# Kernel tuning notes

Hardware: AMD Instinct MI355X
Metric: run time of the kernel (lower is better)

## Reference

```python
import jax, jax.numpy as jnp
import numpy as np

M, N = 4096, 4096
N_COEF = 768
ALPHA = 16.0


def _dct_mat(K):
    # Orthonormal DCT-II matrix D: D[k, t] = s(k) * cos(pi * (t + 0.5) * k / K)
    # dct2d(X)  = D_M @ X @ D_N.T ;  idct2d(Y) = D_M.T @ Y @ D_N  (DCT-III)
    k = jnp.arange(K, dtype=jnp.float32)[:, None]
    t = jnp.arange(K, dtype=jnp.float32)[None, :]
    D = jnp.cos(jnp.pi * (t + 0.5) * k / K)
    scale = jnp.where(k == 0, jnp.sqrt(1.0 / K), jnp.sqrt(2.0 / K))
    return (D * scale).astype(jnp.float32)


def setup_inputs() -> dict:
    key = jax.random.key(0)
    k1, k2, k3 = jax.random.split(key, 3)
    weight = jax.random.normal(k1, (M, N), dtype=jnp.float32) * 0.02
    dW_params = jax.random.normal(k2, (N_COEF,), dtype=jnp.float32) * 0.05
    flat_indices = jax.random.randint(k3, (N_COEF,), 0, M * N, dtype=jnp.int64)
    return {"weight": weight, "dW_params": dW_params, "flat_indices": flat_indices}


def reference(weight, dW_params, flat_indices):
    # W_eff = stop_grad(W) + idct2d(scatter(dW_params)) * alpha
    m, n = weight.shape
    dW_F = jnp.zeros(m * n, dtype=jnp.float32).at[flat_indices].set(dW_params)
    dW_F = dW_F.reshape(m, n)
    D_M = _dct_mat(m)
    D_N = _dct_mat(n)
    dW_T = D_M.T @ dW_F @ D_N  # dense 2D inverse DCT (DCT-III)
    return jax.lax.stop_gradient(weight) + dW_T * ALPHA
```

## Files before the change

kernel.cpp:

```cpp
#include <hip/hip_runtime.h>

#define MDIM 4096
#define NDIM 4096
#define NCOEF 768
#define ALPHA 16.0f
#define PANEL_U16 (96 * 256 * 8)

typedef __attribute__((ext_vector_type(8))) short bf16x8;
typedef __attribute__((ext_vector_type(4))) float f32x4;

__device__ __forceinline__ unsigned short f2bf(float x) {
    unsigned u = __float_as_uint(x);
    u += 0x7FFFu + ((u >> 16) & 1u);
    return (unsigned short)(u >> 16);
}

__device__ __forceinline__ void glds16(const unsigned short* src, unsigned short* dst) {
    __builtin_amdgcn_global_load_lds(
        (const __attribute__((address_space(1))) void*)src,
        (__attribute__((address_space(3))) void*)dst, 16, 0, 0);
}

__global__ __launch_bounds__(256) void fill_uv(
    const int* __restrict__ fidx, const float* __restrict__ dw,
    unsigned short* __restrict__ U, unsigned short* __restrict__ V)
{
    __shared__ int idx_s[NCOEF];
    __shared__ int dup[8];
    const int b = blockIdx.x;
    const int half = b & 1;
    const int pk = b >> 1;
    const int panel = pk / 96;
    const int kc = pk - panel * 96;
    const int t = threadIdx.x;
    #pragma unroll
    for (int j = 0; j < 3; ++j) idx_s[t + (j << 8)] = fidx[t + (j << 8)];
    if (t < 8) dup[t] = 0;
    __syncthreads();
    {
        const int ci = t >> 5;
        const int pci = (kc << 3) + ci;
        const int myidx = idx_s[pci];
        const int q0 = (t & 31) * 24;
        int found = 0;
        #pragma unroll
        for (int s = 0; s < 24; ++s) {
            const int q = q0 + s;
            found |= (q > pci) & (idx_s[q] == myidx);
        }
        if (found) dup[ci] = 1;
    }
    __syncthreads();
    const int rl = (half << 7) + (t >> 1);
    const int row = (panel << 8) + rl;
    const int p0 = (kc << 3) + ((t & 1) << 2);
    const unsigned tt = 2u * (unsigned)row + 1u;
    const float wrev = 1.0f / 16384.0f;
    const float s0 = 0.015625f;
    const float s1 = 0.022097086912079612f;
    unsigned short uo[4], vo[4];
    #pragma unroll
    for (int j = 0; j < 4; ++j) {
        const int p = p0 + j;
        const int idx = idx_s[p];
        const int r = idx >> 12;
        const int c = idx & (NDIM - 1);
        const float su = (r == 0) ? s0 : s1;
        const float sv = (dup[p - (kc << 3)] ? 0.0f : 1.0f) * ALPHA * dw[p]
                         * ((c == 0) ? s0 : s1);
        const unsigned nu = (tt * (unsigned)r) & 16383u;
        const unsigned nv = (tt * (unsigned)c) & 16383u;
        uo[j] = f2bf(su * __builtin_amdgcn_cosf((float)nu * wrev));
        vo[j] = f2bf(sv * __builtin_amdgcn_cosf((float)nv * wrev));
    }
    const size_t o = ((size_t)pk * 256 + rl) * 8 + ((t & 1) << 2);
    *(ushort4*)(U + o) = *(const ushort4*)uo;
    *(ushort4*)(V + o) = *(const ushort4*)vo;
}

__global__ __launch_bounds__(512, 1) void gemm_kernel(
    const float* __restrict__ W,
    const unsigned short* __restrict__ U,
    const unsigned short* __restrict__ V,
    float* __restrict__ out)
{
    __shared__ unsigned short SM[65536];
    unsigned short* const As = SM;
    unsigned short* const Bs = SM + 32768;

    const int tid = threadIdx.x;
    const int lane = tid & 63;
    const int wave = tid >> 6;

    const int bid = blockIdx.x;
    const int xcd = bid & 7;
    const int local = bid >> 3;
    const int by = ((xcd >> 1) << 2) + (local >> 3);
    const int bx = ((xcd & 1) << 3) + (local & 7);
    const int wr = wave >> 2;
    const int wc = wave & 3;
    const int fr = lane & 15;
    const int fks = lane >> 4;

    const unsigned short* uPan = U + (size_t)by * PANEL_U16;
    const unsigned short* vPan = V + (size_t)bx * PANEL_U16;

    f32x4 acc[8][4] = {};

    const int aO = (((fks << 8) + wr * 128 + fr) << 3);
    const int bO = (((fks << 8) + wc * 64 + fr) << 3);

    const int bcol = (bx << 8) + (lane << 2);
    const int erowBase = (by << 8);
    float4 wA[2][4];
    float4 wB[2][4];

#define STAGE(j, buf) do {                                                  \
        const unsigned short* uS = uPan + (size_t)(j) * 8192;               \
        const unsigned short* vS = vPan + (size_t)(j) * 8192;               \
        glds16(uS + ((size_t)tid << 3),        &As[(buf) * 8192 + (wave << 9)]); \
        glds16(uS + 4096 + ((size_t)tid << 3), &As[(buf) * 8192 + 4096 + (wave << 9)]); \
        glds16(vS + ((size_t)tid << 3),        &Bs[(buf) * 8192 + (wave << 9)]); \
        glds16(vS + 4096 + ((size_t)tid << 3), &Bs[(buf) * 8192 + 4096 + (wave << 9)]); \
    } while (0)

#define COMPUTE(buf) do {                                                   \
        bf16x8 a[8], b[4];                                                  \
        _Pragma("unroll")                                                   \
        for (int fm = 0; fm < 8; ++fm)                                      \
            a[fm] = *(const bf16x8*)&As[(buf) * 8192 + aO + (fm << 7)];     \
        _Pragma("unroll")                                                   \
        for (int fn = 0; fn < 4; ++fn)                                      \
            b[fn] = *(const bf16x8*)&Bs[(buf) * 8192 + bO + (fn << 7)];     \
        _Pragma("unroll")                                                   \
        for (int fm = 0; fm < 8; ++fm)                                      \
            _Pragma("unroll")                                               \
            for (int fn = 0; fn < 4; ++fn)                                  \
                acc[fm][fn] = __builtin_amdgcn_mfma_f32_16x16x32_bf16(      \
                    b[fn], a[fm], acc[fm][fn], 0, 0, 0);                    \
    } while (0)

    STAGE(0, 0);
    STAGE(1, 1);
    #pragma unroll
    for (int j = 0; j < 24; ++j) {
        if (j < 22) STAGE(j + 2, (j + 2) & 3);
        if (j == 21) {
            #pragma unroll
            for (int cc = 0; cc < 2; ++cc)
                #pragma unroll
                for (int i = 0; i < 4; ++i)
                    wA[cc][i] = *(const float4*)(
                        W + (size_t)(erowBase + cc * 32 + wave * 4 + i) * NDIM + bcol);
        }
        if (j < 21)       asm volatile("s_waitcnt vmcnt(8)"  ::: "memory");
        else if (j == 21) asm volatile("s_waitcnt vmcnt(16)" ::: "memory");
        else if (j == 22) asm volatile("s_waitcnt vmcnt(12)" ::: "memory");
        else              asm volatile("s_waitcnt vmcnt(8)"  ::: "memory");
        __builtin_amdgcn_s_barrier();
        asm volatile("" ::: "memory");
        COMPUTE(j & 3);
    }

    float* const L = (float*)SM;
    if (wr == 0) {
        #pragma unroll
        for (int f2 = 0; f2 < 2; ++f2)
            #pragma unroll
            for (int fn = 0; fn < 4; ++fn)
                *(f32x4*)(L + (f2 * 16 + fr) * 258 + wc * 64 + fn * 16 + fks * 4)
                    = acc[f2][fn];
    }
    #pragma unroll
    for (int c = 0; c < 8; ++c) {
        asm volatile("s_waitcnt lgkmcnt(0)" ::: "memory");
        __builtin_amdgcn_s_barrier();
        asm volatile("" ::: "memory");
        if (c < 7) {
            if (wr == ((c + 1) >> 2)) {
                #pragma unroll
                for (int f2 = 0; f2 < 2; ++f2)
                    #pragma unroll
                    for (int fn = 0; fn < 4; ++fn)
                        *(f32x4*)(L + ((c + 1) & 1) * 8256
                                  + (f2 * 16 + fr) * 258 + wc * 64 + fn * 16 + fks * 4)
                            = acc[((c + 1) & 3) * 2 + f2][fn];
            }
        }
        #pragma unroll
        for (int i = 0; i < 4; ++i) {
            const int rl2 = wave * 4 + i;
            const size_t o = (size_t)(erowBase + c * 32 + rl2) * NDIM + bcol;
            const f32x4 l4 = *(const f32x4*)(L + (c & 1) * 8256 + rl2 * 258 + (lane << 2));
            const float4 w4 = (c < 2) ? wA[c][i] : wB[c & 1][i];
            float4 r4;
            r4.x = w4.x + l4[0];
            r4.y = w4.y + l4[1];
            r4.z = w4.z + l4[2];
            r4.w = w4.w + l4[3];
            *(float4*)(out + o) = r4;
        }
        if (c < 6) {
            #pragma unroll
            for (int i = 0; i < 4; ++i)
                wB[c & 1][i] = *(const float4*)(
                    W + (size_t)(erowBase + (c + 2) * 32 + wave * 4 + i) * NDIM + bcol);
        }
    }
#undef STAGE
#undef COMPUTE
}

extern "C" void kernel_launch(void* const* d_in, const int* in_sizes, int n_in,
                              void* d_out, int out_size, void* d_ws, size_t ws_size,
                              hipStream_t stream) {
    const float* weight = (const float*)d_in[0];
    const float* dw     = (const float*)d_in[1];
    const int*   fidx   = (const int*)d_in[2];
    float* out = (float*)d_out;

    char* ws = (char*)d_ws;
    unsigned short* U = (unsigned short*)ws;
    unsigned short* V = (unsigned short*)(ws + 6291456);

    fill_uv<<<16 * 96 * 2, 256, 0, stream>>>(fidx, weight ? (const float*)d_in[1] : (const float*)d_in[1], U, V);
    gemm_kernel<<<256, 512, 0, stream>>>(weight, U, V, out);
}
```

Before: 51.29 us.

## Split GEMM tiles to 256x128 with two blocks per CU and double buffering

The GEMM kernel now uses 256-thread blocks on 256x128 output tiles instead of 512-thread blocks on 256x256, with 512 blocks launched and two blocks per CU. LDS is cut to double buffering (from quad) so that two blocks fit, and an extra barrier per k-step is added. The epilogue is restructured to stage one 32-row chunk at a time, with W prefetch reorganized across threads. This aims to raise occupancy and improve load balance, at the cost of more barriers, less prefetch depth and more redundant U loads across blocks.

After: 48.89 us. 1.05x faster.

```diff
diff --git a/kernel.cpp b/kernel.cpp
--- a/kernel.cpp
+++ b/kernel.cpp
@@ -78,15 +78,15 @@
     *(ushort4*)(V + o) = *(const ushort4*)vo;
 }
 
-__global__ __launch_bounds__(512, 1) void gemm_kernel(
+__global__ __launch_bounds__(256, 2) void gemm_kernel(
     const float* __restrict__ W,
     const unsigned short* __restrict__ U,
     const unsigned short* __restrict__ V,
     float* __restrict__ out)
 {
-    __shared__ unsigned short SM[65536];
+    __shared__ unsigned short SM[24576];
     unsigned short* const As = SM;
-    unsigned short* const Bs = SM + 32768;
+    unsigned short* const Bs = SM + 16384;
 
     const int tid = threadIdx.x;
     const int lane = tid & 63;
@@ -95,116 +95,121 @@
     const int bid = blockIdx.x;
     const int xcd = bid & 7;
     const int local = bid >> 3;
-    const int by = ((xcd >> 1) << 2) + (local >> 3);
-    const int bx = ((xcd & 1) << 3) + (local & 7);
-    const int wr = wave >> 2;
-    const int wc = wave & 3;
+    const int by = ((xcd >> 1) << 2) + (local >> 4);
+    const int bx = ((xcd & 1) << 4) + (local & 15);
+    const int wr = wave >> 1;
+    const int wc = wave & 1;
     const int fr = lane & 15;
     const int fks = lane >> 4;
 
     const unsigned short* uPan = U + (size_t)by * PANEL_U16;
-    const unsigned short* vPan = V + (size_t)bx * PANEL_U16;
+    const unsigned short* vBase = V + (size_t)(bx >> 1) * PANEL_U16
+                                    + (size_t)(bx & 1) * 1024;
 
     f32x4 acc[8][4] = {};
 
     const int aO = (((fks << 8) + wr * 128 + fr) << 3);
-    const int bO = (((fks << 8) + wc * 64 + fr) << 3);
-
-    const int bcol = (bx << 8) + (lane << 2);
-    const int erowBase = (by << 8);
-    float4 wA[2][4];
-    float4 wB[2][4];
-
-#define STAGE(j, buf) do {                                                  \
-        const unsigned short* uS = uPan + (size_t)(j) * 8192;               \
-        const unsigned short* vS = vPan + (size_t)(j) * 8192;               \
-        glds16(uS + ((size_t)tid << 3),        &As[(buf) * 8192 + (wave << 9)]); \
-        glds16(uS + 4096 + ((size_t)tid << 3), &As[(buf) * 8192 + 4096 + (wave << 9)]); \
-        glds16(vS + ((size_t)tid << 3),        &Bs[(buf) * 8192 + (wave << 9)]); \
-        glds16(vS + 4096 + ((size_t)tid << 3), &Bs[(buf) * 8192 + 4096 + (wave << 9)]); \
+    const int bO = (((fks << 7) + wc * 64 + fr) << 3);
+
+    const int bcol = bx << 7;
+    const int erowBase = by << 8;
+    float4 wpre[2][4];
+
+#define STAGE(j, buf) do {                                                   \
+        const unsigned short* uS = uPan + (size_t)(j) * 8192;                \
+        const unsigned short* vS = vBase + (size_t)(j) * 8192;               \
+        _Pragma("unroll")                                                    \
+        for (int q = 0; q < 4; ++q)                                          \
+            glds16(uS + (((q << 8) + tid) << 3),                             \
+                   &As[(buf) * 8192 + ((q << 11) + (wave << 9))]);           \
+        _Pragma("unroll")                                                    \
+        for (int q = 0; q < 2; ++q) {                                        \
+            const int c = (q << 8) + tid;                                    \
+            glds16(vS + ((c + ((c >> 7) << 7)) << 3),                        \
+                   &Bs[(buf) * 4096 + ((q << 11) + (wave << 9))]);           \
+        }                                                                    \
     } while (0)
 
-#define COMPUTE(buf) do {                                                   \
-        bf16x8 a[8], b[4];                                                  \
-        _Pragma("unroll")                                                   \
-        for (int fm = 0; fm < 8; ++fm)                                      \
-            a[fm] = *(const bf16x8*)&As[(buf) * 8192 + aO + (fm << 7)];     \
-        _Pragma("unroll")                                                   \
-        for (int fn = 0; fn < 4; ++fn)                                      \
-            b[fn] = *(const bf16x8*)&Bs[(buf) * 8192 + bO + (fn << 7)];     \
-        _Pragma("unroll")                                                   \
-        for (int fm = 0; fm < 8; ++fm)                                      \
-            _Pragma("unroll")                                               \
-            for (int fn = 0; fn < 4; ++fn)                                  \
-                acc[fm][fn] = __builtin_amdgcn_mfma_f32_16x16x32_bf16(      \
-                    b[fn], a[fm], acc[fm][fn], 0, 0, 0);                    \
+#define COMPUTE(buf) do {                                                    \
+        bf16x8 a[8], b[4];                                                   \
+        _Pragma("unroll")                                                    \
+        for (int fm = 0; fm < 8; ++fm)                                       \
+            a[fm] = *(const bf16x8*)&As[(buf) * 8192 + aO + (fm << 7)];      \
+        _Pragma("unroll")                                                    \
+        for (int fn = 0; fn < 4; ++fn)                                       \
+            b[fn] = *(const bf16x8*)&Bs[(buf) * 4096 + bO + (fn << 7)];      \
+        _Pragma("unroll")                                                    \
+        for (int fm = 0; fm < 8; ++fm)                                       \
+            _Pragma("unroll")                                                \
+            for (int fn = 0; fn < 4; ++fn)                                   \
+                acc[fm][fn] = __builtin_amdgcn_mfma_f32_16x16x32_bf16(       \
+                    b[fn], a[fm], acc[fm][fn], 0, 0, 0);                     \
     } while (0)
 
     STAGE(0, 0);
-    STAGE(1, 1);
     #pragma unroll
     for (int j = 0; j < 24; ++j) {
-        if (j < 22) STAGE(j + 2, (j + 2) & 3);
-        if (j == 21) {
+        if (j < 23) STAGE(j + 1, (j + 1) & 1);
+        if (j == 22) {
             #pragma unroll
-            for (int cc = 0; cc < 2; ++cc)
-                #pragma unroll
-                for (int i = 0; i < 4; ++i)
-                    wA[cc][i] = *(const float4*)(
-                        W + (size_t)(erowBase + cc * 32 + wave * 4 + i) * NDIM + bcol);
-        }
-        if (j < 21)       asm volatile("s_waitcnt vmcnt(8)"  ::: "memory");
-        else if (j == 21) asm volatile("s_waitcnt vmcnt(16)" ::: "memory");
-        else if (j == 22) asm volatile("s_waitcnt vmcnt(12)" ::: "memory");
-        else              asm volatile("s_waitcnt vmcnt(8)"  ::: "memory");
+            for (int i = 0; i < 4; ++i) {
+                const int idx = (i << 8) + tid;
+                wpre[0][i] = *(const float4*)(
+                    W + (size_t)(erowBase + (idx >> 5)) * NDIM + bcol + ((idx & 31) << 2));
+            }
+        }
+        if (j < 22)       asm volatile("s_waitcnt vmcnt(6)"  ::: "memory");
+        else if (j == 22) asm volatile("s_waitcnt vmcnt(10)" ::: "memory");
+        else              asm volatile("s_waitcnt vmcnt(4)"  ::: "memory");
         __builtin_amdgcn_s_barrier();
         asm volatile("" ::: "memory");
-        COMPUTE(j & 3);
+        COMPUTE(j & 1);
+        if (j < 23) {
+            asm volatile("s_waitcnt lgkmcnt(0)" ::: "memory");
+            __builtin_amdgcn_s_barrier();
+            asm volatile("" ::: "memory");
+        }
     }
 
     float* const L = (float*)SM;
-    if (wr == 0) {
-        #pragma unroll
-        for (int f2 = 0; f2 < 2; ++f2)
-            #pragma unroll
-            for (int fn = 0; fn < 4; ++fn)
-                *(f32x4*)(L + (f2 * 16 + fr) * 258 + wc * 64 + fn * 16 + fks * 4)
-                    = acc[f2][fn];
-    }
     #pragma unroll
     for (int c = 0; c < 8; ++c) {
         asm volatile("s_waitcnt lgkmcnt(0)" ::: "memory");
         __builtin_amdgcn_s_barrier();
         asm volatile("" ::: "memory");
+        if (wr == (c >> 2)) {
+            #pragma unroll
+            for (int f2 = 0; f2 < 2; ++f2)
+                #pragma unroll
+                for (int fn = 0; fn < 4; ++fn)
+                    *(f32x4*)(L + (f2 * 16 + fr) * 132 + wc * 64 + fn * 16 + fks * 4)
+                        = acc[(c & 3) * 2 + f2][fn];
+        }
         if (c < 7) {
-            if (wr == ((c + 1) >> 2)) {
-                #pragma unroll
-                for (int f2 = 0; f2 < 2; ++f2)
-                    #pragma unroll
-                    for (int fn = 0; fn < 4; ++fn)
-                        *(f32x4*)(L + ((c + 1) & 1) * 8256
-                                  + (f2 * 16 + fr) * 258 + wc * 64 + fn * 16 + fks * 4)
-                            = acc[((c + 1) & 3) * 2 + f2][fn];
+            #pragma unroll
+            for (int i = 0; i < 4; ++i) {
+                const int idx = (i << 8) + tid;
+                wpre[(c + 1) & 1][i] = *(const float4*)(
+                    W + (size_t)(erowBase + (c + 1) * 32 + (idx >> 5)) * NDIM
+                      + bcol + ((idx & 31) << 2));
             }
         }
+        asm volatile("s_waitcnt lgkmcnt(0)" ::: "memory");
+        __builtin_amdgcn_s_barrier();
+        asm volatile("" ::: "memory");
         #pragma unroll
         for (int i = 0; i < 4; ++i) {
-            const int rl2 = wave * 4 + i;
-            const size_t o = (size_t)(erowBase + c * 32 + rl2) * NDIM + bcol;
-            const f32x4 l4 = *(const f32x4*)(L + (c & 1) * 8256 + rl2 * 258 + (lane << 2));
-            const float4 w4 = (c < 2) ? wA[c][i] : wB[c & 1][i];
+            const int idx = (i << 8) + tid;
+            const int rl = idx >> 5;
+            const int c4 = (idx & 31) << 2;
+            const size_t o = (size_t)(erowBase + c * 32 + rl) * NDIM + bcol + c4;
+            const f32x4 l4 = *(const f32x4*)(L + rl * 132 + c4);
             float4 r4;
-            r4.x = w4.x + l4[0];
-            r4.y = w4.y + l4[1];
-            r4.z = w4.z + l4[2];
-            r4.w = w4.w + l4[3];
+            r4.x = wpre[c & 1][i].x + l4[0];
+            r4.y = wpre[c & 1][i].y + l4[1];
+            r4.z = wpre[c & 1][i].z + l4[2];
+            r4.w = wpre[c & 1][i].w + l4[3];
             *(float4*)(out + o) = r4;
-        }
-        if (c < 6) {
-            #pragma unroll
-            for (int i = 0; i < 4; ++i)
-                wB[c & 1][i] = *(const float4*)(
-                    W + (size_t)(erowBase + (c + 2) * 32 + wave * 4 + i) * NDIM + bcol);
         }
     }
 #undef STAGE
@@ -223,6 +228,6 @@
     unsigned short* U = (unsigned short*)ws;
     unsigned short* V = (unsigned short*)(ws + 6291456);
 
-    fill_uv<<<16 * 96 * 2, 256, 0, stream>>>(fidx, weight ? (const float*)d_in[1] : (const float*)d_in[1], U, V);
-    gemm_kernel<<<256, 512, 0, stream>>>(weight, U, V, out);
-}
+    fill_uv<<<16 * 96 * 2, 256, 0, stream>>>(fidx, dw, U, V);
+    gemm_kernel<<<512, 256, 0, stream>>>(weight, U, V, out);
+}
```

## Prefetch early weight rows into LDS during GEMM main loop with double buffering

Applied to the files above, without the earlier changes.

Shrinks the U/V staging ring from four buffers to two and uses the freed LDS to prefetch the first 64 rows of the weight tile through global_load_lds during the first eight k-iterations. The intent is to overlap the epilogue's weight reads with compute and so shorten the output phase. In exchange, the main loop now needs an extra barrier every iteration and has less prefetch depth, and the epilogue gains an extra barrier per chunk because the L staging area is no longer double-buffered.

New measurement: 51.76 us. No clear change (+0.9%).

```diff
diff --git a/kernel.cpp b/kernel.cpp
--- a/kernel.cpp
+++ b/kernel.cpp
@@ -86,7 +86,8 @@
 {
     __shared__ unsigned short SM[65536];
     unsigned short* const As = SM;
-    unsigned short* const Bs = SM + 32768;
+    unsigned short* const Bs = SM + 16384;
+    unsigned short* const Wl = SM + 32768;
 
     const int tid = threadIdx.x;
     const int lane = tid & 63;
@@ -140,59 +141,76 @@
                     b[fn], a[fm], acc[fm][fn], 0, 0, 0);                    \
     } while (0)
 
+#define VW(n) asm volatile("s_waitcnt vmcnt(" #n ")" ::: "memory")
+
     STAGE(0, 0);
-    STAGE(1, 1);
     #pragma unroll
     for (int j = 0; j < 24; ++j) {
-        if (j < 22) STAGE(j + 2, (j + 2) & 3);
+        if (j < 23) STAGE(j + 1, (j + 1) & 1);
         if (j == 21) {
             #pragma unroll
-            for (int cc = 0; cc < 2; ++cc)
+            for (int k = 0; k < 2; ++k)
                 #pragma unroll
                 for (int i = 0; i < 4; ++i)
-                    wA[cc][i] = *(const float4*)(
-                        W + (size_t)(erowBase + cc * 32 + wave * 4 + i) * NDIM + bcol);
-        }
-        if (j < 21)       asm volatile("s_waitcnt vmcnt(8)"  ::: "memory");
-        else if (j == 21) asm volatile("s_waitcnt vmcnt(16)" ::: "memory");
-        else if (j == 22) asm volatile("s_waitcnt vmcnt(12)" ::: "memory");
-        else              asm volatile("s_waitcnt vmcnt(8)"  ::: "memory");
+                    wA[k][i] = *(const float4*)(
+                        W + (size_t)(erowBase + (k + 2) * 32 + wave * 4 + i) * NDIM + bcol);
+        }
+        if (j == 0)       VW(4);
+        else if (j <= 8)  VW(5);
+        else if (j <= 21) VW(4);
+        else if (j == 22) VW(12);
+        else              VW(0);
         __builtin_amdgcn_s_barrier();
         asm volatile("" ::: "memory");
-        COMPUTE(j & 3);
+        COMPUTE(j & 1);
+        if (j < 8) {
+            glds16((const unsigned short*)(W + (size_t)(erowBase + j * 8 + wave) * NDIM
+                                             + (bx << 8)) + ((size_t)lane << 3),
+                   &Wl[j * 4096 + (wave << 9)]);
+        }
+        if (j < 23) {
+            asm volatile("s_waitcnt lgkmcnt(0)" ::: "memory");
+            __builtin_amdgcn_s_barrier();
+            asm volatile("" ::: "memory");
+        }
     }
 
     float* const L = (float*)SM;
-    if (wr == 0) {
-        #pragma unroll
-        for (int f2 = 0; f2 < 2; ++f2)
-            #pragma unroll
-            for (int fn = 0; fn < 4; ++fn)
-                *(f32x4*)(L + (f2 * 16 + fr) * 258 + wc * 64 + fn * 16 + fks * 4)
-                    = acc[f2][fn];
-    }
     #pragma unroll
     for (int c = 0; c < 8; ++c) {
         asm volatile("s_waitcnt lgkmcnt(0)" ::: "memory");
         __builtin_amdgcn_s_barrier();
         asm volatile("" ::: "memory");
-        if (c < 7) {
-            if (wr == ((c + 1) >> 2)) {
+        if (wr == (c >> 2)) {
+            #pragma unroll
+            for (int f2 = 0; f2 < 2; ++f2)
                 #pragma unroll
-                for (int f2 = 0; f2 < 2; ++f2)
-                    #pragma unroll
-                    for (int fn = 0; fn < 4; ++fn)
-                        *(f32x4*)(L + ((c + 1) & 1) * 8256
-                                  + (f2 * 16 + fr) * 258 + wc * 64 + fn * 16 + fks * 4)
-                            = acc[((c + 1) & 3) * 2 + f2][fn];
-            }
+                for (int fn = 0; fn < 4; ++fn)
+                    *(f32x4*)(L + (f2 * 16 + fr) * 258 + wc * 64 + fn * 16 + fks * 4)
+                        = acc[(c & 3) * 2 + f2][fn];
+        }
+        asm volatile("s_waitcnt lgkmcnt(0)" ::: "memory");
+        __builtin_amdgcn_s_barrier();
+        asm volatile("" ::: "memory");
+        if (c >= 4) {
+            if (c < 7) VW(8);
+            else       VW(4);
         }
         #pragma unroll
         for (int i = 0; i < 4; ++i) {
             const int rl2 = wave * 4 + i;
             const size_t o = (size_t)(erowBase + c * 32 + rl2) * NDIM + bcol;
-            const f32x4 l4 = *(const f32x4*)(L + (c & 1) * 8256 + rl2 * 258 + (lane << 2));
-            const float4 w4 = (c < 2) ? wA[c][i] : wB[c & 1][i];
+            float4 w4;
+            if (c < 2) {
+                const float* wlds = (const float*)Wl;
+                const f32x4 wv = *(const f32x4*)(wlds + (c * 32 + rl2) * 256 + (lane << 2));
+                w4.x = wv[0]; w4.y = wv[1]; w4.z = wv[2]; w4.w = wv[3];
+            } else if (c < 4) {
+                w4 = wA[c - 2][i];
+            } else {
+                w4 = wB[c & 1][i];
+            }
+            const f32x4 l4 = *(const f32x4*)(L + rl2 * 258 + (lane << 2));
             float4 r4;
             r4.x = w4.x + l4[0];
             r4.y = w4.y + l4[1];
@@ -200,7 +218,7 @@
             r4.w = w4.w + l4[3];
             *(float4*)(out + o) = r4;
         }
-        if (c < 6) {
+        if (c >= 2 && c < 6) {
             #pragma unroll
             for (int i = 0; i < 4; ++i)
                 wB[c & 1][i] = *(const float4*)(
@@ -209,6 +227,7 @@
     }
 #undef STAGE
 #undef COMPUTE
+#undef VW
 }
 
 extern "C" void kernel_launch(void* const* d_in, const int* in_sizes, int n_in,
@@ -223,6 +242,6 @@
     unsigned short* U = (unsigned short*)ws;
     unsigned short* V = (unsigned short*)(ws + 6291456);
 
-    fill_uv<<<16 * 96 * 2, 256, 0, stream>>>(fidx, weight ? (const float*)d_in[1] : (const float*)d_in[1], U, V);
+    fill_uv<<<16 * 96 * 2, 256, 0, stream>>>(fidx, dw, U, V);
     gemm_kernel<<<256, 512, 0, stream>>>(weight, U, V, out);
 }
```

## Restructure GEMM main loop into ping-pong quarter-tile phases with setprio

Applied to the files above, without the earlier changes.

The K loop is split into finer phases: each 32-wide K step is handled as two half-M MFMA quarters, with global-to-LDS loads for A and B issued separately and interleaved with LDS reads, bracketed by barriers and s_setprio around the MFMA bursts. The weight prefetch for the epilogue is reorganised so only the first chunk is loaded during the last iteration and later chunks are loaded one step ahead inside the epilogue. The aim is better overlap of memory traffic with MFMA work and smoother wave scheduling. It adds many more barriers per iteration and leaves less distance for hiding the epilogue weight loads.

After: 52.04 us. No clear change (+1.5%).

```diff
diff --git a/kernel.cpp b/kernel.cpp
--- a/kernel.cpp
+++ b/kernel.cpp
@@ -106,60 +106,79 @@
     const unsigned short* vPan = V + (size_t)bx * PANEL_U16;
 
     f32x4 acc[8][4] = {};
+    bf16x8 aQ[4], bb[4];
 
     const int aO = (((fks << 8) + wr * 128 + fr) << 3);
     const int bO = (((fks << 8) + wc * 64 + fr) << 3);
 
     const int bcol = (bx << 8) + (lane << 2);
     const int erowBase = (by << 8);
-    float4 wA[2][4];
-    float4 wB[2][4];
-
-#define STAGE(j, buf) do {                                                  \
-        const unsigned short* uS = uPan + (size_t)(j) * 8192;               \
-        const unsigned short* vS = vPan + (size_t)(j) * 8192;               \
+    float4 wpre[2][4];
+
+#define SGA(kt, buf) do {                                                   \
+        const unsigned short* uS = uPan + (size_t)(kt) * 8192;              \
         glds16(uS + ((size_t)tid << 3),        &As[(buf) * 8192 + (wave << 9)]); \
         glds16(uS + 4096 + ((size_t)tid << 3), &As[(buf) * 8192 + 4096 + (wave << 9)]); \
+    } while (0)
+#define SGB(kt, buf) do {                                                   \
+        const unsigned short* vS = vPan + (size_t)(kt) * 8192;              \
         glds16(vS + ((size_t)tid << 3),        &Bs[(buf) * 8192 + (wave << 9)]); \
         glds16(vS + 4096 + ((size_t)tid << 3), &Bs[(buf) * 8192 + 4096 + (wave << 9)]); \
     } while (0)
-
-#define COMPUTE(buf) do {                                                   \
-        bf16x8 a[8], b[4];                                                  \
+#define DSA(buf, base) do {                                                 \
         _Pragma("unroll")                                                   \
-        for (int fm = 0; fm < 8; ++fm)                                      \
-            a[fm] = *(const bf16x8*)&As[(buf) * 8192 + aO + (fm << 7)];     \
+        for (int f = 0; f < 4; ++f)                                         \
+            aQ[f] = *(const bf16x8*)&As[(buf) * 8192 + aO + (((base) + f) << 7)]; \
+    } while (0)
+#define DSB(buf) do {                                                       \
         _Pragma("unroll")                                                   \
-        for (int fn = 0; fn < 4; ++fn)                                      \
-            b[fn] = *(const bf16x8*)&Bs[(buf) * 8192 + bO + (fn << 7)];     \
+        for (int f = 0; f < 4; ++f)                                         \
+            bb[f] = *(const bf16x8*)&Bs[(buf) * 8192 + bO + (f << 7)];      \
+    } while (0)
+#define MFMAQ(fmb) do {                                                     \
+        __builtin_amdgcn_s_setprio(1);                                      \
         _Pragma("unroll")                                                   \
-        for (int fm = 0; fm < 8; ++fm)                                      \
+        for (int fm = 0; fm < 4; ++fm)                                      \
             _Pragma("unroll")                                               \
             for (int fn = 0; fn < 4; ++fn)                                  \
-                acc[fm][fn] = __builtin_amdgcn_mfma_f32_16x16x32_bf16(      \
-                    b[fn], a[fm], acc[fm][fn], 0, 0, 0);                    \
-    } while (0)
-
-    STAGE(0, 0);
-    STAGE(1, 1);
-    #pragma unroll
-    for (int j = 0; j < 24; ++j) {
-        if (j < 22) STAGE(j + 2, (j + 2) & 3);
-        if (j == 21) {
-            #pragma unroll
-            for (int cc = 0; cc < 2; ++cc)
-                #pragma unroll
-                for (int i = 0; i < 4; ++i)
-                    wA[cc][i] = *(const float4*)(
-                        W + (size_t)(erowBase + cc * 32 + wave * 4 + i) * NDIM + bcol);
-        }
-        if (j < 21)       asm volatile("s_waitcnt vmcnt(8)"  ::: "memory");
-        else if (j == 21) asm volatile("s_waitcnt vmcnt(16)" ::: "memory");
-        else if (j == 22) asm volatile("s_waitcnt vmcnt(12)" ::: "memory");
-        else              asm volatile("s_waitcnt vmcnt(8)"  ::: "memory");
-        __builtin_amdgcn_s_barrier();
-        asm volatile("" ::: "memory");
-        COMPUTE(j & 3);
+                acc[(fmb) + fm][fn] = __builtin_amdgcn_mfma_f32_16x16x32_bf16( \
+                    bb[fn], aQ[fm], acc[(fmb) + fm][fn], 0, 0, 0);          \
+        __builtin_amdgcn_s_setprio(0);                                      \
+    } while (0)
+#define BAR()  __builtin_amdgcn_s_barrier()
+#define LGKM() do { asm volatile("s_waitcnt lgkmcnt(0)" ::: "memory");      \
+                    __builtin_amdgcn_sched_barrier(0); } while (0)
+#define VW4()  asm volatile("s_waitcnt vmcnt(4)" ::: "memory")
+
+    SGA(0, 0); SGB(0, 0); SGA(1, 1); SGB(1, 1);
+    VW4();
+    BAR();
+
+    #pragma unroll
+    for (int j = 0; j < 12; ++j) {
+        const int b0 = (2 * j) & 3, b1 = (2 * j + 1) & 3;
+        const int n0 = (2 * j + 2) & 3, n1 = (2 * j + 3) & 3;
+        DSA(b0, 0); DSB(b0);
+        if (j < 11) { SGA(2 * j + 2, n0); }
+        else {
+            wpre[0][0] = *(const float4*)(W + (size_t)(erowBase + wave * 4 + 0) * NDIM + bcol);
+            wpre[0][1] = *(const float4*)(W + (size_t)(erowBase + wave * 4 + 1) * NDIM + bcol);
+        }
+        BAR(); LGKM(); MFMAQ(0); BAR();
+        DSA(b0, 4);
+        if (j < 11) { SGB(2 * j + 2, n0); }
+        else {
+            wpre[0][2] = *(const float4*)(W + (size_t)(erowBase + wave * 4 + 2) * NDIM + bcol);
+            wpre[0][3] = *(const float4*)(W + (size_t)(erowBase + wave * 4 + 3) * NDIM + bcol);
+        }
+        VW4();
+        BAR(); LGKM(); MFMAQ(4); BAR();
+        DSA(b1, 0); DSB(b1);
+        if (j < 11) SGA(2 * j + 3, n1);
+        BAR(); LGKM(); MFMAQ(0); BAR();
+        DSA(b1, 4);
+        if (j < 11) { SGB(2 * j + 3, n1); VW4(); }
+        BAR(); LGKM(); MFMAQ(4); BAR();
     }
 
     float* const L = (float*)SM;
@@ -173,10 +192,12 @@
     }
     #pragma unroll
     for (int c = 0; c < 8; ++c) {
-        asm volatile("s_waitcnt lgkmcnt(0)" ::: "memory");
-        __builtin_amdgcn_s_barrier();
-        asm volatile("" ::: "memory");
+        __syncthreads();
         if (c < 7) {
+            #pragma unroll
+            for (int i = 0; i < 4; ++i)
+                wpre[(c + 1) & 1][i] = *(const float4*)(
+                    W + (size_t)(erowBase + (c + 1) * 32 + wave * 4 + i) * NDIM + bcol);
             if (wr == ((c + 1) >> 2)) {
                 #pragma unroll
                 for (int f2 = 0; f2 < 2; ++f2)
@@ -192,23 +213,22 @@
             const int rl2 = wave * 4 + i;
             const size_t o = (size_t)(erowBase + c * 32 + rl2) * NDIM + bcol;
             const f32x4 l4 = *(const f32x4*)(L + (c & 1) * 8256 + rl2 * 258 + (lane << 2));
-            const float4 w4 = (c < 2) ? wA[c][i] : wB[c & 1][i];
             float4 r4;
-            r4.x = w4.x + l4[0];
-            r4.y = w4.y + l4[1];
-            r4.z = w4.z + l4[2];
-            r4.w = w4.w + l4[3];
+            r4.x = wpre[c & 1][i].x + l4[0];
+            r4.y = wpre[c & 1][i].y + l4[1];
+            r4.z = wpre[c & 1][i].z + l4[2];
+            r4.w = wpre[c & 1][i].w + l4[3];
             *(float4*)(out + o) = r4;
         }
-        if (c < 6) {
-            #pragma unroll
-            for (int i = 0; i < 4; ++i)
-                wB[c & 1][i] = *(const float4*)(
-                    W + (size_t)(erowBase + (c + 2) * 32 + wave * 4 + i) * NDIM + bcol);
-        }
-    }
-#undef STAGE
-#undef COMPUTE
+    }
+#undef SGA
+#undef SGB
+#undef DSA
+#undef DSB
+#undef MFMAQ
+#undef BAR
+#undef LGKM
+#undef VW4
 }
 
 extern "C" void kernel_launch(void* const* d_in, const int* in_sizes, int n_in,
@@ -223,6 +243,6 @@
     unsigned short* U = (unsigned short*)ws;
     unsigned short* V = (unsigned short*)(ws + 6291456);
 
-    fill_uv<<<16 * 96 * 2, 256, 0, stream>>>(fidx, weight ? (const float*)d_in[1] : (const float*)d_in[1], U, V);
+    fill_uv<<<16 * 96 * 2, 256, 0, stream>>>(fidx, dw, U, V);
     gemm_kernel<<<256, 512, 0, stream>>>(weight, U, V, out);
 }
```
